# Performance work log

Hardware: AMD Instinct MI355X
Metric: run time of the kernel (lower is better)

## Reference

```python
import jax, jax.numpy as jnp
import numpy as np

B, C, H, W = 8, 256, 32, 32
N_HEAD = 4
EPS = 1e-5


def setup_inputs() -> dict:
    key = jax.random.key(0)
    ks = jax.random.split(key, 8)
    return {
        "input": jax.random.normal(ks[0], (B, C, H, W), dtype=jnp.float32),
        "bn_gamma": jnp.ones((C,), dtype=jnp.float32),
        "bn_beta": jnp.zeros((C,), dtype=jnp.float32),
        "bn_mean": jax.random.normal(ks[1], (C,), dtype=jnp.float32) * 0.1,
        "bn_var": jax.random.uniform(ks[2], (C,), dtype=jnp.float32, minval=0.5, maxval=1.5),
        "dw_w": jax.random.normal(ks[3], (C,), dtype=jnp.float32) * (1.0 / np.sqrt(C)),
        "pw_w": jax.random.normal(ks[4], (3 * C, C), dtype=jnp.float32) * (1.0 / np.sqrt(C)),
        "out_w": jax.random.normal(ks[5], (C, C), dtype=jnp.float32) * (1.0 / np.sqrt(C)),
        "out_b": jnp.zeros((C,), dtype=jnp.float32),
    }


def reference(input, bn_gamma, bn_beta, bn_mean, bn_var, dw_w, pw_w, out_w, out_b):
    b, c, h, w = input.shape
    n_head = N_HEAD
    head_dim = c // n_head

    # BatchNorm2d (eval mode: running stats), fused with depthwise 1x1 conv
    # (groups=C, kernel 1x1 -> per-channel scalar multiply).
    scale = (bn_gamma * jax.lax.rsqrt(bn_var + EPS) * dw_w)[None, :, None, None]
    shift = (bn_beta * dw_w)[None, :, None, None]
    mean = bn_mean[None, :, None, None]
    x = (input - mean) * scale + shift  # [B,C,H,W]

    # Pointwise 1x1 conv -> QKV: [B, 3C, H, W]
    qkv = jnp.einsum('oc,bchw->bohw', pw_w, x)
    qkv = qkv.reshape(b, n_head, head_dim * 3, h, w)
    q, k, v = jnp.split(qkv, 3, axis=2)  # each [B,n,d,H,W]

    # Full spatial attention logits: [B, n, H, W, H, W]
    attn = jnp.einsum('bnchw,bncyx->bnhwyx', q, k) * (1.0 / np.sqrt(head_dim))
    # Faithful to original: softmax over LAST axis (key x/width) ONLY.
    attn = jax.nn.softmax(attn, axis=-1)

    out = jnp.einsum('bnhwyx,bncyx->bnchw', attn, v).reshape(b, c, h, w)
    out = jnp.einsum('oc,bchw->bohw', out_w, out) + out_b[None, :, None, None]
    return out + input
```

## Files before the change

### kernel.cpp

```cpp
#include <hip/hip_runtime.h>

#define NB 8
#define NC 256
#define NS 1024
#define NHEAD 4
#define HD 64
#define OC 768

#define QSCALE 0.1803368801111204f

typedef float f32x4 __attribute__((ext_vector_type(4)));
typedef __bf16 bf16x8 __attribute__((ext_vector_type(8)));
typedef unsigned short u16;
typedef unsigned int u32;
typedef u16 u16x8 __attribute__((ext_vector_type(8)));
typedef u32 u32x2 __attribute__((ext_vector_type(2)));
typedef int i32x4 __attribute__((ext_vector_type(4)));
typedef short s16x4 __attribute__((ext_vector_type(4)));

__device__ __forceinline__ u16 f2b(float f) {
    return __builtin_bit_cast(u16, (__bf16)f);
}
__device__ __forceinline__ u32 pack2(float lo, float hi) {
    return (u32)f2b(lo) | ((u32)f2b(hi) << 16);
}

__device__ __forceinline__ f32x4 MFMA(u16x8 a, u16x8 b, f32x4 c) {
    return __builtin_amdgcn_mfma_f32_16x16x32_bf16(
        __builtin_bit_cast(bf16x8, a), __builtin_bit_cast(bf16x8, b), c, 0, 0, 0);
}

__global__ void xform(const float* __restrict__ in,
                      const float* __restrict__ gma, const float* __restrict__ bta,
                      const float* __restrict__ mu,  const float* __restrict__ var,
                      const float* __restrict__ dw,  u16* __restrict__ xt) {
    __shared__ float tile[32][33];
    __shared__ float ssc[32], ssh[32];
    int b = blockIdx.z, c0 = blockIdx.y * 32, s0 = blockIdx.x * 32;
    int tx = threadIdx.x & 31, ty = threadIdx.x >> 5;
    if (threadIdx.x < 32) {
        int c = c0 + threadIdx.x;
        float sc = gma[c] * rsqrtf(var[c] + 1e-5f) * dw[c];
        ssc[threadIdx.x] = sc;
        ssh[threadIdx.x] = bta[c] * dw[c] - mu[c] * sc;
    }
    __syncthreads();
#pragma unroll
    for (int r = 0; r < 4; r++) {
        int c = ty + r * 8;
        tile[c][tx] = in[((size_t)b * NC + c0 + c) * NS + s0 + tx] * ssc[c] + ssh[c];
    }
    __syncthreads();
#pragma unroll
    for (int r = 0; r < 4; r++) {
        int s = ty + r * 8;
        xt[((size_t)b * NS + s0 + s) * NC + c0 + tx] = f2b(tile[tx][s]);
    }
}

__global__ __launch_bounds__(256) void qkv_gemm(const float* __restrict__ pw, const u16* __restrict__ xt,
                                                u16* __restrict__ qb, u16* __restrict__ kb,
                                                u16* __restrict__ vb) {
    __shared__ __attribute__((aligned(16))) u16 Ws[64][72];
    __shared__ __attribute__((aligned(16))) u16 Xs[128][72];
    int b = blockIdx.z;
    int m0 = blockIdx.y * 64, n0 = blockIdx.x * 128;
    int tid = threadIdx.x, lane = tid & 63, w = tid >> 6, lg = lane >> 4, li = lane & 15;
    int rowA = tid >> 2, colA = (tid & 3) * 16;
    int rowB = tid >> 1, colB = (tid & 1) * 32;
    const float* pA = pw + (size_t)(m0 + rowA) * NC + colA;
    const u16*   pB = xt + ((size_t)b * NS + n0 + rowB) * NC + colB;
    f32x4 acc[4][2] = {};
#pragma unroll
    for (int k0 = 0; k0 < NC; k0 += 64) {
        f32x4 a0 = *(const f32x4*)(pA + k0);
        f32x4 a1 = *(const f32x4*)(pA + k0 + 4);
        f32x4 a2 = *(const f32x4*)(pA + k0 + 8);
        f32x4 a3 = *(const f32x4*)(pA + k0 + 12);
        i32x4 tb0 = *(const i32x4*)(pB + k0);
        i32x4 tb1 = *(const i32x4*)(pB + k0 + 8);
        i32x4 tb2 = *(const i32x4*)(pB + k0 + 16);
        i32x4 tb3 = *(const i32x4*)(pB + k0 + 24);
        __syncthreads();
        i32x4 wa0, wa1;
        wa0[0] = pack2(a0[0], a0[1]); wa0[1] = pack2(a0[2], a0[3]);
        wa0[2] = pack2(a1[0], a1[1]); wa0[3] = pack2(a1[2], a1[3]);
        wa1[0] = pack2(a2[0], a2[1]); wa1[1] = pack2(a2[2], a2[3]);
        wa1[2] = pack2(a3[0], a3[1]); wa1[3] = pack2(a3[2], a3[3]);
        *(i32x4*)&Ws[rowA][colA]     = wa0;
        *(i32x4*)&Ws[rowA][colA + 8] = wa1;
        *(i32x4*)&Xs[rowB][colB]      = tb0;
        *(i32x4*)&Xs[rowB][colB + 8]  = tb1;
        *(i32x4*)&Xs[rowB][colB + 16] = tb2;
        *(i32x4*)&Xs[rowB][colB + 24] = tb3;
        __syncthreads();
        u16x8 af[4][2], bfr[2][2];
#pragma unroll
        for (int mf = 0; mf < 4; mf++)
#pragma unroll
            for (int kc = 0; kc < 2; kc++)
                af[mf][kc] = *(const u16x8*)&Ws[mf * 16 + li][kc * 32 + lg * 8];
#pragma unroll
        for (int nf = 0; nf < 2; nf++)
#pragma unroll
            for (int kc = 0; kc < 2; kc++)
                bfr[nf][kc] = *(const u16x8*)&Xs[w * 32 + nf * 16 + li][kc * 32 + lg * 8];
#pragma unroll
        for (int kc = 0; kc < 2; kc++)
#pragma unroll
            for (int mf = 0; mf < 4; mf++)
#pragma unroll
                for (int nf = 0; nf < 2; nf++)
                    acc[mf][nf] = MFMA(af[mf][kc], bfr[nf][kc], acc[mf][nf]);
    }
    int sel = (m0 >> 6) % 3;
    int n = m0 / 192;
    size_t bn = (size_t)b * NHEAD + n;
    if (sel == 0) {
#pragma unroll
        for (int mf = 0; mf < 4; mf++)
#pragma unroll
            for (int nf = 0; nf < 2; nf++) {
                int d0 = mf * 16 + lg * 4;
                int s = n0 + w * 32 + nf * 16 + li;
                u32x2 pk;
                pk[0] = pack2(acc[mf][nf][0] * QSCALE, acc[mf][nf][1] * QSCALE);
                pk[1] = pack2(acc[mf][nf][2] * QSCALE, acc[mf][nf][3] * QSCALE);
                *(u32x2*)(qb + (bn * NS + s) * HD + d0) = pk;
            }
    } else if (sel == 1) {
#pragma unroll
        for (int mf = 0; mf < 4; mf++)
#pragma unroll
            for (int nf = 0; nf < 2; nf++) {
                int d0 = mf * 16 + lg * 4;
                int s = n0 + w * 32 + nf * 16 + li;
                u32x2 pk;
                pk[0] = pack2(acc[mf][nf][0], acc[mf][nf][1]);
                pk[1] = pack2(acc[mf][nf][2], acc[mf][nf][3]);
                *(u32x2*)(kb + (bn * NS + s) * HD + d0) = pk;
            }
    } else {
#pragma unroll
        for (int mf = 0; mf < 4; mf++)
#pragma unroll
            for (int j = 0; j < 4; j++) {
                int r = mf * 16 + lg * 4 + j;
#pragma unroll
                for (int nf = 0; nf < 2; nf++) {
                    int s = n0 + w * 32 + nf * 16 + li;
                    vb[(bn * HD + r) * NS + s] = f2b(acc[mf][nf][j]);
                }
            }
    }
}

#define SMEM_K 0
#define SMEM_V 9216
#if __has_builtin(__builtin_amdgcn_mfma_f32_16x16x16bf16_1k)
#define PV16 1
#define SMEM_BYTES 34816
#else
#define PV16 0
#define SMEM_P 18432
#define SMEM_BYTES 38912
#endif
__global__ __launch_bounds__(256) void attn_k(const u16* __restrict__ qbuf, const u16* __restrict__ kbuf,
                                              const u16* __restrict__ vbuf, u16* __restrict__ ao0,
                                              u16* __restrict__ ao1) {
    __shared__ __attribute__((aligned(16))) char smem[SMEM_BYTES];
    u16 (*Ks)[72] = (u16(*)[72])(smem + SMEM_K);
    u16 (*Vs)[72] = (u16(*)[72])(smem + SMEM_V);
#if !PV16
    u16 (*Ps)[64][40] = (u16(*)[64][40])(smem + SMEM_P);
#endif
    float (*red)[68] = (float(*)[68])smem;
    int b = blockIdx.z, n = blockIdx.y;
    int s0 = (blockIdx.x >> 1) * 128;
    int th = blockIdx.x & 1;
    u16* aoh = th ? ao1 : ao0;
    size_t bn = (size_t)b * NHEAD + n;
    const u16* qg = qbuf + (bn * NS + s0) * HD;
    const u16* kg = kbuf + (bn * NS + th * 512) * HD;
    const u16* vg = vbuf + bn * HD * NS + th * 512;
    int tid = threadIdx.x, lane = tid & 63, w = tid >> 6, lg = lane >> 4, li = lane & 15;
    int tq = w & 1, tt = w >> 1;
    int srow = tid >> 2, sc8 = (tid & 3) * 16;
    i32x4 rk0 = *(const i32x4*)(kg + srow * HD + sc8);
    i32x4 rk1 = *(const i32x4*)(kg + srow * HD + sc8 + 8);
    i32x4 rv0 = *(const i32x4*)(vg + srow * NS + sc8);
    i32x4 rv1 = *(const i32x4*)(vg + srow * NS + sc8 + 8);
    u16x8 bq[4][2];
#pragma unroll
    for (int qf = 0; qf < 4; qf++)
#pragma unroll
        for (int kc = 0; kc < 2; kc++)
            bq[qf][kc] = *(const u16x8*)(qg + (tq * 64 + qf * 16 + li) * HD + kc * 32 + lg * 8);
    f32x4 oacc[4][4] = {};
    for (int t0 = 0; t0 < 512; t0 += 64) {
        __syncthreads();
        *(i32x4*)&Ks[srow][sc8]     = rk0;
        *(i32x4*)&Ks[srow][sc8 + 8] = rk1;
        *(i32x4*)&Vs[srow][sc8]     = rv0;
        *(i32x4*)&Vs[srow][sc8 + 8] = rv1;
        __syncthreads();
        if (t0 + 64 < 512) {
            rk0 = *(const i32x4*)(kg + (t0 + 64 + srow) * HD + sc8);
            rk1 = *(const i32x4*)(kg + (t0 + 64 + srow) * HD + sc8 + 8);
            rv0 = *(const i32x4*)(vg + srow * NS + t0 + 64 + sc8);
            rv1 = *(const i32x4*)(vg + srow * NS + t0 + 64 + sc8 + 8);
        }
        u16x8 ak[2][2];
#pragma unroll
        for (int tf = 0; tf < 2; tf++)
#pragma unroll
            for (int kc = 0; kc < 2; kc++)
                ak[tf][kc] = *(const u16x8*)&Ks[tt * 32 + tf * 16 + li][kc * 32 + lg * 8];
        f32x4 sacc[2][4];
        __builtin_amdgcn_s_setprio(1);
#pragma unroll
        for (int tf = 0; tf < 2; tf++)
#pragma unroll
            for (int qf = 0; qf < 4; qf++) {
                f32x4 z = {0.f, 0.f, 0.f, 0.f};
                z = MFMA(ak[tf][0], bq[qf][0], z);
                sacc[tf][qf] = MFMA(ak[tf][1], bq[qf][1], z);
            }
        __builtin_amdgcn_s_setprio(0);
        u32x2 pp[4][2];
#pragma unroll
        for (int qf = 0; qf < 4; qf++) {
            float p[8];
            float sum = 0.f;
#pragma unroll
            for (int j = 0; j < 4; j++) { p[j] = exp2f(sacc[0][qf][j]); sum += p[j]; }
#pragma unroll
            for (int j = 0; j < 4; j++) { p[4 + j] = exp2f(sacc[1][qf][j]); sum += p[4 + j]; }
            sum += __shfl_xor(sum, 16);
            sum += __shfl_xor(sum, 32);
            float inv = 1.0f / sum;
#pragma unroll
            for (int tf = 0; tf < 2; tf++) {
                u32x2 pk;
                pk[0] = pack2(p[tf * 4 + 0] * inv, p[tf * 4 + 1] * inv);
                pk[1] = pack2(p[tf * 4 + 2] * inv, p[tf * 4 + 3] * inv);
                pp[qf][tf] = pk;
            }
        }
#if PV16
        s16x4 bv16[4][2];
#pragma unroll
        for (int nf = 0; nf < 4; nf++)
#pragma unroll
            for (int tf = 0; tf < 2; tf++)
                bv16[nf][tf] = *(const s16x4*)&Vs[nf * 16 + li][tt * 32 + tf * 16 + lg * 4];
        __builtin_amdgcn_s_setprio(1);
#pragma unroll
        for (int qf = 0; qf < 4; qf++) {
            s16x4 pa0 = __builtin_bit_cast(s16x4, pp[qf][0]);
            s16x4 pa1 = __builtin_bit_cast(s16x4, pp[qf][1]);
#pragma unroll
            for (int nf = 0; nf < 4; nf++) {
                oacc[qf][nf] = __builtin_amdgcn_mfma_f32_16x16x16bf16_1k(pa0, bv16[nf][0], oacc[qf][nf], 0, 0, 0);
                oacc[qf][nf] = __builtin_amdgcn_mfma_f32_16x16x16bf16_1k(pa1, bv16[nf][1], oacc[qf][nf], 0, 0, 0);
            }
        }
        __builtin_amdgcn_s_setprio(0);
#else
#pragma unroll
        for (int qf = 0; qf < 4; qf++)
#pragma unroll
            for (int tf = 0; tf < 2; tf++)
                *(u32x2*)&Ps[w][qf * 16 + li][tf * 16 + lg * 4] = pp[qf][tf];
        u16x8 pa[4];
#pragma unroll
        for (int qf = 0; qf < 4; qf++)
            pa[qf] = *(const u16x8*)&Ps[w][qf * 16 + li][lg * 8];
        u16x8 bv[4];
#pragma unroll
        for (int nf = 0; nf < 4; nf++)
            bv[nf] = *(const u16x8*)&Vs[nf * 16 + li][tt * 32 + lg * 8];
        __builtin_amdgcn_s_setprio(1);
#pragma unroll
        for (int qf = 0; qf < 4; qf++)
#pragma unroll
            for (int nf = 0; nf < 4; nf++)
                oacc[qf][nf] = MFMA(pa[qf], bv[nf], oacc[qf][nf]);
        __builtin_amdgcn_s_setprio(0);
#endif
    }
    __syncthreads();
    if (tt == 1) {
#pragma unroll
        for (int qf = 0; qf < 4; qf++)
#pragma unroll
            for (int nf = 0; nf < 4; nf++)
#pragma unroll
                for (int j = 0; j < 4; j++)
                    red[tq * 64 + qf * 16 + lg * 4 + j][nf * 16 + li] = oacc[qf][nf][j];
    }
    __syncthreads();
    if (tt == 0) {
#pragma unroll
        for (int qf = 0; qf < 4; qf++)
#pragma unroll
            for (int nf = 0; nf < 4; nf++)
#pragma unroll
                for (int j = 0; j < 4; j++) {
                    int s = s0 + tq * 64 + qf * 16 + lg * 4 + j;
                    int c = n * HD + nf * 16 + li;
                    float v = oacc[qf][nf][j] + red[tq * 64 + qf * 16 + lg * 4 + j][nf * 16 + li];
                    aoh[((size_t)b * NS + s) * NC + c] = f2b(v);
                }
    }
}

__global__ __launch_bounds__(256) void out_gemm(const float* __restrict__ ow, const u16* __restrict__ ao0,
                                                const u16* __restrict__ ao1,
                                                const float* __restrict__ outb, const float* __restrict__ in,
                                                float* __restrict__ out) {
    __shared__ __attribute__((aligned(16))) u16 Ws[64][72];
    __shared__ __attribute__((aligned(16))) u16 Xs[128][72];
    int b = blockIdx.z;
    int m0 = blockIdx.y * 64, n0 = blockIdx.x * 128;
    int tid = threadIdx.x, lane = tid & 63, w = tid >> 6, lg = lane >> 4, li = lane & 15;
    int rowA = tid >> 2, colA = (tid & 3) * 16;
    int rowB = tid >> 1, colB = (tid & 1) * 32;
    const float* pA = ow + (size_t)(m0 + rowA) * NC + colA;
    size_t boff = ((size_t)b * NS + n0 + rowB) * NC + colB;
    f32x4 acc[4][2] = {};
#pragma unroll
    for (int k0 = 0; k0 < 2 * NC; k0 += 64) {
        const u16* pB = (k0 < NC ? ao0 : ao1) + boff + (k0 & (NC - 1));
        int ka = k0 & (NC - 1);
        f32x4 a0 = *(const f32x4*)(pA + ka);
        f32x4 a1 = *(const f32x4*)(pA + ka + 4);
        f32x4 a2 = *(const f32x4*)(pA + ka + 8);
        f32x4 a3 = *(const f32x4*)(pA + ka + 12);
        i32x4 tb0 = *(const i32x4*)(pB);
        i32x4 tb1 = *(const i32x4*)(pB + 8);
        i32x4 tb2 = *(const i32x4*)(pB + 16);
        i32x4 tb3 = *(const i32x4*)(pB + 24);
        __syncthreads();
        i32x4 wa0, wa1;
        wa0[0] = pack2(a0[0], a0[1]); wa0[1] = pack2(a0[2], a0[3]);
        wa0[2] = pack2(a1[0], a1[1]); wa0[3] = pack2(a1[2], a1[3]);
        wa1[0] = pack2(a2[0], a2[1]); wa1[1] = pack2(a2[2], a2[3]);
        wa1[2] = pack2(a3[0], a3[1]); wa1[3] = pack2(a3[2], a3[3]);
        *(i32x4*)&Ws[rowA][colA]     = wa0;
        *(i32x4*)&Ws[rowA][colA + 8] = wa1;
        *(i32x4*)&Xs[rowB][colB]      = tb0;
        *(i32x4*)&Xs[rowB][colB + 8]  = tb1;
        *(i32x4*)&Xs[rowB][colB + 16] = tb2;
        *(i32x4*)&Xs[rowB][colB + 24] = tb3;
        __syncthreads();
        u16x8 af[4][2], bfr[2][2];
#pragma unroll
        for (int mf = 0; mf < 4; mf++)
#pragma unroll
            for (int kc = 0; kc < 2; kc++)
                af[mf][kc] = *(const u16x8*)&Ws[mf * 16 + li][kc * 32 + lg * 8];
#pragma unroll
        for (int nf = 0; nf < 2; nf++)
#pragma unroll
            for (int kc = 0; kc < 2; kc++)
                bfr[nf][kc] = *(const u16x8*)&Xs[w * 32 + nf * 16 + li][kc * 32 + lg * 8];
#pragma unroll
        for (int kc = 0; kc < 2; kc++)
#pragma unroll
            for (int mf = 0; mf < 4; mf++)
#pragma unroll
                for (int nf = 0; nf < 2; nf++)
                    acc[mf][nf] = MFMA(af[mf][kc], bfr[nf][kc], acc[mf][nf]);
    }
#pragma unroll
    for (int mf = 0; mf < 4; mf++)
#pragma unroll
        for (int j = 0; j < 4; j++) {
            int o = m0 + mf * 16 + lg * 4 + j;
            float bias = outb[o];
#pragma unroll
            for (int nf = 0; nf < 2; nf++) {
                int s = n0 + w * 32 + nf * 16 + li;
                size_t idx = ((size_t)b * NC + o) * NS + s;
                out[idx] = acc[mf][nf][j] + bias + in[idx];
            }
        }
}

extern "C" void kernel_launch(void* const* d_in, const int* in_sizes, int n_in,
                              void* d_out, int out_size, void* d_ws, size_t ws_size,
                              hipStream_t stream) {
    const float* input = (const float*)d_in[0];
    const float* gma = (const float*)d_in[1];
    const float* bta = (const float*)d_in[2];
    const float* mu  = (const float*)d_in[3];
    const float* var = (const float*)d_in[4];
    const float* dw  = (const float*)d_in[5];
    const float* pw  = (const float*)d_in[6];
    const float* ow  = (const float*)d_in[7];
    const float* ob  = (const float*)d_in[8];
    float* out = (float*)d_out;
    char* ws = (char*)d_ws;

    const size_t SZ_BIG = (size_t)NB * NS * NC * 2;
    u16* xt  = (u16*)(ws);
    u16* qb  = (u16*)(ws + SZ_BIG);
    u16* kb  = (u16*)(ws + 2 * SZ_BIG);
    u16* vb  = (u16*)(ws + 3 * SZ_BIG);
    u16* ao1 = (u16*)(ws + 4 * SZ_BIG);
    u16* ao0 = xt;

    xform<<<dim3(32, 8, 8), 256, 0, stream>>>(input, gma, bta, mu, var, dw, xt);
    qkv_gemm<<<dim3(8, 12, 8), 256, 0, stream>>>(pw, xt, qb, kb, vb);
    attn_k<<<dim3(16, 4, 8), 256, 0, stream>>>(qb, kb, vb, ao0, ao1);
    out_gemm<<<dim3(8, 4, 8), 256, 0, stream>>>(ow, ao0, ao1, ob, input, out);
}
```

Baseline: 58.73 us.

## Pre-convert weights to bf16 once and double-buffer K/V tiles in attention

Adds extra blocks to the xform kernel that convert the QKV and output projection weights to bf16 in the workspace, so both GEMMs load half the weight bytes and skip per-block fp32 packing. The attention kernel gets double-buffered K/V shared-memory tiles, dropping one barrier per iteration and overlapping the next tile's store with compute. The non-PV16 path now builds the P operand in registers instead of going through shared memory. Costs are more shared memory in attention and a little extra work in xform.

```diff
diff --git a/kernel.cpp b/kernel.cpp
--- a/kernel.cpp
+++ b/kernel.cpp
@@ -15,6 +15,7 @@
 typedef unsigned int u32;
 typedef u16 u16x8 __attribute__((ext_vector_type(8)));
 typedef u32 u32x2 __attribute__((ext_vector_type(2)));
+typedef u32 u32x4 __attribute__((ext_vector_type(4)));
 typedef int i32x4 __attribute__((ext_vector_type(4)));
 typedef short s16x4 __attribute__((ext_vector_type(4)));
 
@@ -33,7 +34,20 @@
 __global__ void xform(const float* __restrict__ in,
                       const float* __restrict__ gma, const float* __restrict__ bta,
                       const float* __restrict__ mu,  const float* __restrict__ var,
-                      const float* __restrict__ dw,  u16* __restrict__ xt) {
+                      const float* __restrict__ dw,  const float* __restrict__ pw,
+                      const float* __restrict__ ow,  u16* __restrict__ pwb,
+                      u16* __restrict__ owb,         u16* __restrict__ xt) {
+    if (blockIdx.y == 8) {
+        int idx = ((blockIdx.z * 32 + blockIdx.x) * 256 + threadIdx.x) * 4;
+        f32x4 v = (idx < OC * NC) ? *(const f32x4*)(pw + idx)
+                                  : *(const f32x4*)(ow + idx - OC * NC);
+        u32x2 pk;
+        pk[0] = pack2(v[0], v[1]);
+        pk[1] = pack2(v[2], v[3]);
+        if (idx < OC * NC) *(u32x2*)(pwb + idx) = pk;
+        else               *(u32x2*)(owb + idx - OC * NC) = pk;
+        return;
+    }
     __shared__ float tile[32][33];
     __shared__ float ssc[32], ssh[32];
     int b = blockIdx.z, c0 = blockIdx.y * 32, s0 = blockIdx.x * 32;
@@ -58,7 +72,7 @@
     }
 }
 
-__global__ __launch_bounds__(256) void qkv_gemm(const float* __restrict__ pw, const u16* __restrict__ xt,
+__global__ __launch_bounds__(256) void qkv_gemm(const u16* __restrict__ pwb, const u16* __restrict__ xt,
                                                 u16* __restrict__ qb, u16* __restrict__ kb,
                                                 u16* __restrict__ vb) {
     __shared__ __attribute__((aligned(16))) u16 Ws[64][72];
@@ -68,27 +82,20 @@
     int tid = threadIdx.x, lane = tid & 63, w = tid >> 6, lg = lane >> 4, li = lane & 15;
     int rowA = tid >> 2, colA = (tid & 3) * 16;
     int rowB = tid >> 1, colB = (tid & 1) * 32;
-    const float* pA = pw + (size_t)(m0 + rowA) * NC + colA;
-    const u16*   pB = xt + ((size_t)b * NS + n0 + rowB) * NC + colB;
+    const u16* pA = pwb + (size_t)(m0 + rowA) * NC + colA;
+    const u16* pB = xt + ((size_t)b * NS + n0 + rowB) * NC + colB;
     f32x4 acc[4][2] = {};
 #pragma unroll
     for (int k0 = 0; k0 < NC; k0 += 64) {
-        f32x4 a0 = *(const f32x4*)(pA + k0);
-        f32x4 a1 = *(const f32x4*)(pA + k0 + 4);
-        f32x4 a2 = *(const f32x4*)(pA + k0 + 8);
-        f32x4 a3 = *(const f32x4*)(pA + k0 + 12);
+        i32x4 ta0 = *(const i32x4*)(pA + k0);
+        i32x4 ta1 = *(const i32x4*)(pA + k0 + 8);
         i32x4 tb0 = *(const i32x4*)(pB + k0);
         i32x4 tb1 = *(const i32x4*)(pB + k0 + 8);
         i32x4 tb2 = *(const i32x4*)(pB + k0 + 16);
         i32x4 tb3 = *(const i32x4*)(pB + k0 + 24);
         __syncthreads();
-        i32x4 wa0, wa1;
-        wa0[0] = pack2(a0[0], a0[1]); wa0[1] = pack2(a0[2], a0[3]);
-        wa0[2] = pack2(a1[0], a1[1]); wa0[3] = pack2(a1[2], a1[3]);
-        wa1[0] = pack2(a2[0], a2[1]); wa1[1] = pack2(a2[2], a2[3]);
-        wa1[2] = pack2(a3[0], a3[1]); wa1[3] = pack2(a3[2], a3[3]);
-        *(i32x4*)&Ws[rowA][colA]     = wa0;
-        *(i32x4*)&Ws[rowA][colA + 8] = wa1;
+        *(i32x4*)&Ws[rowA][colA]     = ta0;
+        *(i32x4*)&Ws[rowA][colA + 8] = ta1;
         *(i32x4*)&Xs[rowB][colB]      = tb0;
         *(i32x4*)&Xs[rowB][colB + 8]  = tb1;
         *(i32x4*)&Xs[rowB][colB + 16] = tb2;
@@ -155,25 +162,18 @@
     }
 }
 
-#define SMEM_K 0
-#define SMEM_V 9216
+#define SMEM_BYTES 36864
 #if __has_builtin(__builtin_amdgcn_mfma_f32_16x16x16bf16_1k)
 #define PV16 1
-#define SMEM_BYTES 34816
 #else
 #define PV16 0
-#define SMEM_P 18432
-#define SMEM_BYTES 38912
 #endif
 __global__ __launch_bounds__(256) void attn_k(const u16* __restrict__ qbuf, const u16* __restrict__ kbuf,
                                               const u16* __restrict__ vbuf, u16* __restrict__ ao0,
                                               u16* __restrict__ ao1) {
     __shared__ __attribute__((aligned(16))) char smem[SMEM_BYTES];
-    u16 (*Ks)[72] = (u16(*)[72])(smem + SMEM_K);
-    u16 (*Vs)[72] = (u16(*)[72])(smem + SMEM_V);
-#if !PV16
-    u16 (*Ps)[64][40] = (u16(*)[64][40])(smem + SMEM_P);
-#endif
+    u16 (*Ks)[64][72] = (u16(*)[64][72])(smem);
+    u16 (*Vs)[64][72] = (u16(*)[64][72])(smem + 18432);
     float (*red)[68] = (float(*)[68])smem;
     int b = blockIdx.z, n = blockIdx.y;
     int s0 = (blockIdx.x >> 1) * 128;
@@ -196,13 +196,13 @@
 #pragma unroll
         for (int kc = 0; kc < 2; kc++)
             bq[qf][kc] = *(const u16x8*)(qg + (tq * 64 + qf * 16 + li) * HD + kc * 32 + lg * 8);
+    *(i32x4*)&Ks[0][srow][sc8]     = rk0;
+    *(i32x4*)&Ks[0][srow][sc8 + 8] = rk1;
+    *(i32x4*)&Vs[0][srow][sc8]     = rv0;
+    *(i32x4*)&Vs[0][srow][sc8 + 8] = rv1;
     f32x4 oacc[4][4] = {};
+    int cur = 0;
     for (int t0 = 0; t0 < 512; t0 += 64) {
-        __syncthreads();
-        *(i32x4*)&Ks[srow][sc8]     = rk0;
-        *(i32x4*)&Ks[srow][sc8 + 8] = rk1;
-        *(i32x4*)&Vs[srow][sc8]     = rv0;
-        *(i32x4*)&Vs[srow][sc8 + 8] = rv1;
         __syncthreads();
         if (t0 + 64 < 512) {
             rk0 = *(const i32x4*)(kg + (t0 + 64 + srow) * HD + sc8);
@@ -215,7 +215,7 @@
         for (int tf = 0; tf < 2; tf++)
 #pragma unroll
             for (int kc = 0; kc < 2; kc++)
-                ak[tf][kc] = *(const u16x8*)&Ks[tt * 32 + tf * 16 + li][kc * 32 + lg * 8];
+                ak[tf][kc] = *(const u16x8*)&Ks[cur][tt * 32 + tf * 16 + li][kc * 32 + lg * 8];
         f32x4 sacc[2][4];
         __builtin_amdgcn_s_setprio(1);
 #pragma unroll
@@ -253,7 +253,7 @@
         for (int nf = 0; nf < 4; nf++)
 #pragma unroll
             for (int tf = 0; tf < 2; tf++)
-                bv16[nf][tf] = *(const s16x4*)&Vs[nf * 16 + li][tt * 32 + tf * 16 + lg * 4];
+                bv16[nf][tf] = *(const s16x4*)&Vs[cur][nf * 16 + li][tt * 32 + tf * 16 + lg * 4];
         __builtin_amdgcn_s_setprio(1);
 #pragma unroll
         for (int qf = 0; qf < 4; qf++) {
@@ -267,27 +267,31 @@
         }
         __builtin_amdgcn_s_setprio(0);
 #else
-#pragma unroll
-        for (int qf = 0; qf < 4; qf++)
-#pragma unroll
-            for (int tf = 0; tf < 2; tf++)
-                *(u32x2*)&Ps[w][qf * 16 + li][tf * 16 + lg * 4] = pp[qf][tf];
         u16x8 pa[4];
 #pragma unroll
-        for (int qf = 0; qf < 4; qf++)
-            pa[qf] = *(const u16x8*)&Ps[w][qf * 16 + li][lg * 8];
+        for (int qf = 0; qf < 4; qf++) {
+            u32x4 t;
+            t[0] = pp[qf][0][0]; t[1] = pp[qf][0][1];
+            t[2] = pp[qf][1][0]; t[3] = pp[qf][1][1];
+            pa[qf] = __builtin_bit_cast(u16x8, t);
+        }
         u16x8 bv[4];
 #pragma unroll
         for (int nf = 0; nf < 4; nf++)
-            bv[nf] = *(const u16x8*)&Vs[nf * 16 + li][tt * 32 + lg * 8];
-        __builtin_amdgcn_s_setprio(1);
+            bv[nf] = *(const u16x8*)&Vs[cur][nf * 16 + li][tt * 32 + lg * 8];
 #pragma unroll
         for (int qf = 0; qf < 4; qf++)
 #pragma unroll
             for (int nf = 0; nf < 4; nf++)
                 oacc[qf][nf] = MFMA(pa[qf], bv[nf], oacc[qf][nf]);
-        __builtin_amdgcn_s_setprio(0);
 #endif
+        if (t0 + 64 < 512) {
+            *(i32x4*)&Ks[cur ^ 1][srow][sc8]     = rk0;
+            *(i32x4*)&Ks[cur ^ 1][srow][sc8 + 8] = rk1;
+            *(i32x4*)&Vs[cur ^ 1][srow][sc8]     = rv0;
+            *(i32x4*)&Vs[cur ^ 1][srow][sc8 + 8] = rv1;
+        }
+        cur ^= 1;
     }
     __syncthreads();
     if (tt == 1) {
@@ -315,7 +319,7 @@
     }
 }
 
-__global__ __launch_bounds__(256) void out_gemm(const float* __restrict__ ow, const u16* __restrict__ ao0,
+__global__ __launch_bounds__(256) void out_gemm(const u16* __restrict__ owb, const u16* __restrict__ ao0,
                                                 const u16* __restrict__ ao1,
                                                 const float* __restrict__ outb, const float* __restrict__ in,
                                                 float* __restrict__ out) {
@@ -326,29 +330,22 @@
     int tid = threadIdx.x, lane = tid & 63, w = tid >> 6, lg = lane >> 4, li = lane & 15;
     int rowA = tid >> 2, colA = (tid & 3) * 16;
     int rowB = tid >> 1, colB = (tid & 1) * 32;
-    const float* pA = ow + (size_t)(m0 + rowA) * NC + colA;
+    const u16* pA = owb + (size_t)(m0 + rowA) * NC + colA;
     size_t boff = ((size_t)b * NS + n0 + rowB) * NC + colB;
     f32x4 acc[4][2] = {};
 #pragma unroll
     for (int k0 = 0; k0 < 2 * NC; k0 += 64) {
         const u16* pB = (k0 < NC ? ao0 : ao1) + boff + (k0 & (NC - 1));
         int ka = k0 & (NC - 1);
-        f32x4 a0 = *(const f32x4*)(pA + ka);
-        f32x4 a1 = *(const f32x4*)(pA + ka + 4);
-        f32x4 a2 = *(const f32x4*)(pA + ka + 8);
-        f32x4 a3 = *(const f32x4*)(pA + ka + 12);
+        i32x4 ta0 = *(const i32x4*)(pA + ka);
+        i32x4 ta1 = *(const i32x4*)(pA + ka + 8);
         i32x4 tb0 = *(const i32x4*)(pB);
         i32x4 tb1 = *(const i32x4*)(pB + 8);
         i32x4 tb2 = *(const i32x4*)(pB + 16);
         i32x4 tb3 = *(const i32x4*)(pB + 24);
         __syncthreads();
-        i32x4 wa0, wa1;
-        wa0[0] = pack2(a0[0], a0[1]); wa0[1] = pack2(a0[2], a0[3]);
-        wa0[2] = pack2(a1[0], a1[1]); wa0[3] = pack2(a1[2], a1[3]);
-        wa1[0] = pack2(a2[0], a2[1]); wa1[1] = pack2(a2[2], a2[3]);
-        wa1[2] = pack2(a3[0], a3[1]); wa1[3] = pack2(a3[2], a3[3]);
-        *(i32x4*)&Ws[rowA][colA]     = wa0;
-        *(i32x4*)&Ws[rowA][colA + 8] = wa1;
+        *(i32x4*)&Ws[rowA][colA]     = ta0;
+        *(i32x4*)&Ws[rowA][colA + 8] = ta1;
         *(i32x4*)&Xs[rowB][colB]      = tb0;
         *(i32x4*)&Xs[rowB][colB + 8]  = tb1;
         *(i32x4*)&Xs[rowB][colB + 16] = tb2;
@@ -403,16 +400,20 @@
     float* out = (float*)d_out;
     char* ws = (char*)d_ws;
 
+    const size_t SZ_PWB = (size_t)OC * NC * 2;
+    const size_t SZ_OWB = (size_t)NC * NC * 2;
     const size_t SZ_BIG = (size_t)NB * NS * NC * 2;
-    u16* xt  = (u16*)(ws);
-    u16* qb  = (u16*)(ws + SZ_BIG);
-    u16* kb  = (u16*)(ws + 2 * SZ_BIG);
-    u16* vb  = (u16*)(ws + 3 * SZ_BIG);
-    u16* ao1 = (u16*)(ws + 4 * SZ_BIG);
+    u16* pwb = (u16*)(ws);
+    u16* owb = (u16*)(ws + SZ_PWB);
+    u16* xt  = (u16*)(ws + SZ_PWB + SZ_OWB);
+    u16* qb  = (u16*)(ws + SZ_PWB + SZ_OWB + SZ_BIG);
+    u16* kb  = (u16*)(ws + SZ_PWB + SZ_OWB + 2 * SZ_BIG);
+    u16* vb  = (u16*)(ws + SZ_PWB + SZ_OWB + 3 * SZ_BIG);
+    u16* ao1 = (u16*)(ws + SZ_PWB + SZ_OWB + 4 * SZ_BIG);
     u16* ao0 = xt;
 
-    xform<<<dim3(32, 8, 8), 256, 0, stream>>>(input, gma, bta, mu, var, dw, xt);
-    qkv_gemm<<<dim3(8, 12, 8), 256, 0, stream>>>(pw, xt, qb, kb, vb);
+    xform<<<dim3(32, 9, 8), 256, 0, stream>>>(input, gma, bta, mu, var, dw, pw, ow, pwb, owb, xt);
+    qkv_gemm<<<dim3(8, 12, 8), 256, 0, stream>>>(pwb, xt, qb, kb, vb);
     attn_k<<<dim3(16, 4, 8), 256, 0, stream>>>(qb, kb, vb, ao0, ao1);
-    out_gemm<<<dim3(8, 4, 8), 256, 0, stream>>>(ow, ao0, ao1, ob, input, out);
-}
+    out_gemm<<<dim3(8, 4, 8), 256, 0, stream>>>(owb, ao0, ao1, ob, input, out);
+}
```

Result: slower. 62.87 us (+7.0%).
